# Performance work log

Measured on AMD Instinct MI355X. Metric: run time of the kernel, lower is better.

## Reference

```python
import jax, jax.numpy as jnp
import numpy as np

B, S, D = 4, 2048, 512
QKD = 256
HID = 3 * D  # expansion_factor=3
EPS = 1e-5


def _ln(x, g, b):
    m = jnp.mean(x, axis=-1, keepdims=True)
    v = jnp.mean((x - m) ** 2, axis=-1, keepdims=True)
    return (x - m) * jax.lax.rsqrt(v + EPS) * g + b


def setup_inputs() -> dict:
    key = jax.random.key(0)
    ks = jax.random.split(key, 12)
    s = lambda fan: 1.0 / np.sqrt(fan)
    return {
        "x":  jax.random.normal(ks[0], (B, S, D), jnp.float32),
        "Wm": jax.random.uniform(ks[1], (D, D), jnp.float32, -s(D), s(D)),
        "bm": jnp.zeros((D,), jnp.float32),
        "g1": jnp.ones((D,), jnp.float32),
        "b1": jnp.zeros((D,), jnp.float32),
        "Wh": jax.random.uniform(ks[2], (2 * HID, D), jnp.float32, -s(D), s(D)),
        "bh": jnp.zeros((2 * HID,), jnp.float32),
        "Wq": jax.random.uniform(ks[3], (QKD, D), jnp.float32, -s(D), s(D)),
        "bq": jnp.zeros((QKD,), jnp.float32),
        "Wb": jax.random.normal(ks[4], (QKD, QKD), jnp.float32),
        "Wo": jax.random.uniform(ks[5], (D, HID), jnp.float32, -s(HID), s(HID)),
        "bo": jnp.zeros((D,), jnp.float32),
        "g2": jnp.ones((D,), jnp.float32),
        "b2": jnp.zeros((D,), jnp.float32),
    }


def reference(x, Wm, bm, g1, b1, Wh, bh, Wq, bq, Wb, Wo, bo, g2, b2):
    seq_len = x.shape[-2]
    memory = jnp.einsum('bsd,ed->bse', x, Wm) + bm
    normed = _ln(x + memory, g1, b1)
    h = jax.nn.relu(jnp.einsum('bsd,hd->bsh', normed, Wh) + bh)
    v, gate = h[..., :HID], h[..., HID:]
    Z = jax.nn.relu(jnp.einsum('bsd,qd->bsq', normed, Wq) + bq)  # [B,S,QKD]
    QK = jnp.einsum('bid,de,bje->bij', Z, Wb, Z) / seq_len
    A = jax.nn.relu(QK) ** 2  # relu^2 attention, no softmax
    V = jnp.einsum('bij,bjd->bid', A, v) * gate
    out = _ln(jnp.einsum('bsh,dh->bsd', V, Wo) + bo, g2, b2)
    return out + x
```

## Files before the change

kernel.cpp:

```cpp
#include <hip/hip_runtime.h>

typedef unsigned short u16;
typedef unsigned char u8;
typedef __attribute__((ext_vector_type(8))) short short8;
typedef __attribute__((ext_vector_type(4))) float f32x4;

#define LN_EPS 1e-5f
#define SCALE_A 4096.f
#define SCALE_V 8.f
#define INV_SCALE_AV (1.f/32768.f)

__device__ __forceinline__ u16 f2bf(float f){
    union { float f; unsigned u; } c; c.f = f;
    unsigned u = c.u + 0x7FFFu + ((c.u >> 16) & 1u);
    return (u16)(u >> 16);
}
__device__ __forceinline__ float bf2f(u16 h){
    union { unsigned u; float f; } c; c.u = ((unsigned)h) << 16;
    return c.f;
}
__device__ __forceinline__ u8 f2fp8(float f){
    int r = __builtin_amdgcn_cvt_pk_fp8_f32(f, 0.f, 0, false);
    return (u8)(r & 0xFF);
}

enum { EPI_NONE=0, EPI_BIAS_RELU, EPI_RELUSQ, EPI_HSPLIT };
enum { OT_F32=0, OT_BF16=1, OT_FP8=2 };

__device__ __forceinline__ void gl2lds16(const void* g, void* lds){
    __builtin_amdgcn_global_load_lds(
        (const __attribute__((address_space(1))) unsigned*)g,
        (__attribute__((address_space(3))) unsigned*)lds, 16, 0, 0);
}

template<int EPI, int OT>
__global__ __launch_bounds__(256)
void mgemm(const u16* __restrict__ A, const u16* __restrict__ B, void* __restrict__ Cv,
           int K, int lda, int ldb, int ldc,
           long sAb, long sBb, long sCb,
           const float* __restrict__ bias,
           const void* __restrict__ ext, int ldext, long sEb,
           float scale, u16* __restrict__ out2, int hsplit)
{
    __shared__ u16 sA[2][4096];
    __shared__ u16 sB[2][4096];
    const int tid = threadIdx.x;
    const int m0 = blockIdx.y * 128, n0 = blockIdx.x * 128;
    const int z  = blockIdx.z;
    const u16* Az = A + (size_t)z * sAb;
    const u16* Bz = B + (size_t)z * sBb;

    const int lane = tid & 63, quad = lane >> 4, l15 = lane & 15;
    const int wave = tid >> 6;
    const int wm = (wave >> 1) * 64, wn = (wave & 1) * 64;

    const u16* gA[2]; const u16* gB[2]; int lo[2];
#pragma unroll
    for (int r = 0; r < 2; r++){
        const int c = tid + r * 256;
        gA[r] = Az + (size_t)(m0 + (c & 127)) * lda + (c >> 7) * 8;
        gB[r] = Bz + (size_t)(n0 + (c & 127)) * ldb + (c >> 7) * 8;
        lo[r] = ((tid & 192) + r * 256) * 16;
    }

    auto stage = [&](int buf, int k0){
#pragma unroll
        for (int r = 0; r < 2; r++){
            gl2lds16(gA[r] + k0, (char*)sA[buf] + lo[r]);
            gl2lds16(gB[r] + k0, (char*)sB[buf] + lo[r]);
        }
    };

    f32x4 acc[4][4];
#pragma unroll
    for (int i = 0; i < 4; i++)
#pragma unroll
        for (int j = 0; j < 4; j++) acc[i][j] = (f32x4){0.f,0.f,0.f,0.f};

    stage(0, 0);
    int buf = 0;
    for (int k0 = 0; k0 < K; k0 += 32){
        __syncthreads();
        if (k0 + 32 < K) stage(buf ^ 1, k0 + 32);
        const u16* fA = sA[buf] + quad * 1024 + (wm + l15) * 8;
        const u16* fB = sB[buf] + quad * 1024 + (wn + l15) * 8;
        short8 a[4], b[4];
#pragma unroll
        for (int t = 0; t < 4; t++){
            a[t] = *(const short8*)(fA + t * 128);
            b[t] = *(const short8*)(fB + t * 128);
        }
#pragma unroll
        for (int i = 0; i < 4; i++)
#pragma unroll
            for (int j = 0; j < 4; j++)
                acc[i][j] = __builtin_amdgcn_mfma_f32_16x16x32_bf16(a[i], b[j], acc[i][j], 0, 0, 0);
        buf ^= 1;
    }

    float* Cf = (float*)Cv; u16* Ch = (u16*)Cv; u8* C8 = (u8*)Cv;
    const size_t zc = (size_t)z * sCb;
#pragma unroll
    for (int i = 0; i < 4; i++){
#pragma unroll
        for (int j = 0; j < 4; j++){
            const int n = n0 + wn + j * 16 + l15;
            float bs = 0.f;
            if (EPI==EPI_BIAS_RELU || EPI==EPI_HSPLIT) bs = bias[n];
#pragma unroll
            for (int r = 0; r < 4; r++){
                const int m = m0 + wm + i * 16 + quad * 4 + r;
                float v = acc[i][j][r] + bs;
                if (EPI==EPI_BIAS_RELU || EPI==EPI_HSPLIT) v = fmaxf(v, 0.f);
                if (EPI==EPI_RELUSQ){ float t = fmaxf(v * scale, 0.f); v = t * t * SCALE_A; }
                if (EPI==EPI_HSPLIT){
                    if (n < hsplit) C8[(size_t)m * ldc + n] = f2fp8(v * SCALE_V);
                    else            out2[(size_t)m * ldc + n - hsplit] = f2bf(v);
                } else if (OT==OT_FP8){
                    C8[zc + (size_t)m * ldc + n] = f2fp8(v);
                } else if (OT==OT_BF16){
                    Ch[zc + (size_t)m * ldc + n] = f2bf(v);
                } else {
                    Cf[zc + (size_t)m * ldc + n] = v;
                }
            }
        }
    }
}

__global__ __launch_bounds__(256)
void mgemm8(const u8* __restrict__ A, const u8* __restrict__ B, u16* __restrict__ C,
            int K, int lda, int ldb, int ldc,
            long sAb, long sBb, long sCb,
            const u16* __restrict__ gate, int ldext, long sEb)
{
    __shared__ u8 sA[2][8192];
    __shared__ u8 sB[2][8192];
    const int tid = threadIdx.x;
    const int m0 = blockIdx.y * 128, n0 = blockIdx.x * 128;
    const int z  = blockIdx.z;
    const u8* Az = A + (size_t)z * sAb;
    const u8* Bz = B + (size_t)z * sBb;

    const int lane = tid & 63, quad = lane >> 4, l15 = lane & 15;
    const int wave = tid >> 6;
    const int wm = (wave >> 1) * 64, wn = (wave & 1) * 64;

    const u8* gA[2]; const u8* gB[2]; int lo[2];
#pragma unroll
    for (int r = 0; r < 2; r++){
        const int c = tid + r * 256;
        gA[r] = Az + (size_t)(m0 + (c & 127)) * lda + (c >> 7) * 16;
        gB[r] = Bz + (size_t)(n0 + (c & 127)) * ldb + (c >> 7) * 16;
        lo[r] = ((tid & 192) + r * 256) * 16;
    }

    auto stage = [&](int buf, int k0){
#pragma unroll
        for (int r = 0; r < 2; r++){
            gl2lds16(gA[r] + k0, (char*)sA[buf] + lo[r]);
            gl2lds16(gB[r] + k0, (char*)sB[buf] + lo[r]);
        }
    };

    f32x4 acc[4][4];
#pragma unroll
    for (int i = 0; i < 4; i++)
#pragma unroll
        for (int j = 0; j < 4; j++) acc[i][j] = (f32x4){0.f,0.f,0.f,0.f};

    stage(0, 0);
    int buf = 0;
    for (int k0 = 0; k0 < K; k0 += 64){
        __syncthreads();
        if (k0 + 64 < K) stage(buf ^ 1, k0 + 64);
#pragma unroll
        for (int t = 0; t < 2; t++){
            const u8* fA = sA[buf] + t * 4096 + (quad >> 1) * 2048 + (wm + l15) * 16 + (quad & 1) * 8;
            const u8* fB = sB[buf] + t * 4096 + (quad >> 1) * 2048 + (wn + l15) * 16 + (quad & 1) * 8;
            long a[4], b[4];
#pragma unroll
            for (int q = 0; q < 4; q++){
                a[q] = *(const long*)(fA + q * 256);
                b[q] = *(const long*)(fB + q * 256);
            }
#pragma unroll
            for (int i = 0; i < 4; i++)
#pragma unroll
                for (int j = 0; j < 4; j++)
                    acc[i][j] = __builtin_amdgcn_mfma_f32_16x16x32_fp8_fp8(a[i], b[j], acc[i][j], 0, 0, 0);
        }
        buf ^= 1;
    }

    const size_t zc = (size_t)z * sCb;
#pragma unroll
    for (int i = 0; i < 4; i++){
#pragma unroll
        for (int j = 0; j < 4; j++){
            const int n = n0 + wn + j * 16 + l15;
#pragma unroll
            for (int r = 0; r < 4; r++){
                const int m = m0 + wm + i * 16 + quad * 4 + r;
                float v = acc[i][j][r] * INV_SCALE_AV
                        * bf2f(gate[(size_t)z * sEb + (size_t)m * ldext + n]);
                C[zc + (size_t)m * ldc + n] = f2bf(v);
            }
        }
    }
}

template<bool OUT_BF, bool POST_RES, int NSUM, bool PRE_RES>
__global__ __launch_bounds__(256)
void ln_k(const float* __restrict__ in, const float* __restrict__ g,
          const float* __restrict__ b, const float* __restrict__ res_post,
          const float* __restrict__ res_pre, const float* __restrict__ bias2,
          long pstride, void* __restrict__ out)
{
    const int row = blockIdx.x, tid = threadIdx.x;
    const size_t base = (size_t)row * 512 + tid * 2;
    float2 v = *(const float2*)(in + base);
#pragma unroll
    for (int p = 1; p < NSUM; p++){
        const float2 w = *(const float2*)(in + (size_t)p * pstride + base);
        v.x += w.x; v.y += w.y;
    }
    if (NSUM > 1){
        const float2 bb2 = *(const float2*)(bias2 + tid * 2);
        v.x += bb2.x; v.y += bb2.y;
    }
    if (PRE_RES){
        const float2 r = *(const float2*)(res_pre + base);
        v.x += r.x; v.y += r.y;
    }
    float s = v.x + v.y, ss = v.x * v.x + v.y * v.y;
#pragma unroll
    for (int off = 32; off > 0; off >>= 1){
        s  += __shfl_down(s,  off);
        ss += __shfl_down(ss, off);
    }
    __shared__ float sbuf[8], ssbuf[8];
    const int wid = tid >> 6, lane = tid & 63;
    if (lane == 0){ sbuf[wid] = s; ssbuf[wid] = ss; }
    __syncthreads();
    if (tid == 0){
        float S = 0.f, SS = 0.f;
#pragma unroll
        for (int i = 0; i < 4; i++){ S += sbuf[i]; SS += ssbuf[i]; }
        const float mean = S * (1.f/512.f);
        const float var  = SS * (1.f/512.f) - mean * mean;
        sbuf[4]  = mean;
        ssbuf[4] = rsqrtf(var + LN_EPS);
    }
    __syncthreads();
    const float mean = sbuf[4], rstd = ssbuf[4];
    const float2 gg = *(const float2*)(g + tid * 2);
    const float2 bb = *(const float2*)(b + tid * 2);
    float ox = (v.x - mean) * rstd * gg.x + bb.x;
    float oy = (v.y - mean) * rstd * gg.y + bb.y;
    if (POST_RES){
        const float2 r = *(const float2*)(res_post + base);
        ox += r.x; oy += r.y;
    }
    if (OUT_BF){
        unsigned pk = ((unsigned)f2bf(oy) << 16) | (unsigned)f2bf(ox);
        ((unsigned*)out)[(size_t)row * 256 + tid] = pk;
    } else {
        *(float2*)((float*)out + base) = make_float2(ox, oy);
    }
}

__global__ __launch_bounds__(256)
void castall_k(const float* __restrict__ x, const float* __restrict__ Wm,
               const float* __restrict__ Wh, const float* __restrict__ Wq,
               const float* __restrict__ Wo, const float* __restrict__ Wb,
               u16* __restrict__ xb, u16* __restrict__ Wmb, u16* __restrict__ Whb,
               u16* __restrict__ Wqb, u16* __restrict__ Wob, u16* __restrict__ WbT)
{
    const int i = blockIdx.x * 256 + threadIdx.x;
    if (i >= 1736704){
        const int j = i - 1736704;
        if (j < 65536){
            const int e = j >> 8, d = j & 255;
            WbT[e * 256 + d] = f2bf(Wb[d * 256 + e]);
        }
        return;
    }
    const float* src; u16* dst; int off;
    if      (i < 1048576){ src = x;  dst = xb;  off = i; }
    else if (i < 1114112){ src = Wm; dst = Wmb; off = i - 1048576; }
    else if (i < 1507328){ src = Wh; dst = Whb; off = i - 1114112; }
    else if (i < 1540096){ src = Wq; dst = Wqb; off = i - 1507328; }
    else                 { src = Wo; dst = Wob; off = i - 1540096; }
    const float4 v = ((const float4*)src)[off];
    ushort4 o; o.x = f2bf(v.x); o.y = f2bf(v.y); o.z = f2bf(v.z); o.w = f2bf(v.w);
    ((ushort4*)dst)[off] = o;
}

__global__ __launch_bounds__(256)
void tr8_k(const u8* __restrict__ v, u8* __restrict__ vT, int S, int HID){
    const int b = blockIdx.z;
    const int h0 = blockIdx.x * 64, s0 = blockIdx.y * 64;
    __shared__ u8 t[64][68];
    const u8* vb = v + (size_t)b * S * HID;
    u8* vTb = vT + (size_t)b * HID * S;
    const int tid = threadIdx.x;
#pragma unroll
    for (int i = 0; i < 4; i++){
        int idx = tid + i * 256;
        int r = idx >> 4, c4 = (idx & 15) * 4;
        uchar4 u = *(const uchar4*)(vb + (size_t)(s0 + r) * HID + h0 + c4);
        t[r][c4] = u.x; t[r][c4+1] = u.y; t[r][c4+2] = u.z; t[r][c4+3] = u.w;
    }
    __syncthreads();
#pragma unroll
    for (int i = 0; i < 4; i++){
        int idx = tid + i * 256;
        int r = idx >> 4, c4 = (idx & 15) * 4;
        uchar4 u;
        u.x = t[c4][r]; u.y = t[c4+1][r]; u.z = t[c4+2][r]; u.w = t[c4+3][r];
        *(uchar4*)(vTb + (size_t)(h0 + r) * S + s0 + c4) = u;
    }
}

extern "C" void kernel_launch(void* const* d_in, const int* in_sizes, int n_in,
                              void* d_out, int out_size, void* d_ws, size_t ws_size,
                              hipStream_t stream)
{
    const float* x  = (const float*)d_in[0];
    const float* Wm = (const float*)d_in[1];
    const float* bm = (const float*)d_in[2];
    const float* g1 = (const float*)d_in[3];
    const float* b1 = (const float*)d_in[4];
    const float* Wh = (const float*)d_in[5];
    const float* bh = (const float*)d_in[6];
    const float* Wq = (const float*)d_in[7];
    const float* bq = (const float*)d_in[8];
    const float* Wb = (const float*)d_in[9];
    const float* Wo = (const float*)d_in[10];
    const float* bo = (const float*)d_in[11];
    const float* g2 = (const float*)d_in[12];
    const float* b2 = (const float*)d_in[13];
    float* out = (float*)d_out;
    (void)in_sizes; (void)n_in; (void)out_size; (void)ws_size;

    const int Bn=4, S=2048, D=512, QKD=256, HID=1536, H2=3072;
    const int M = Bn * S;
    const long MD = (long)M * D;

    char* p = (char*)d_ws;
    auto alloc = [&](size_t bytes)->void*{ void* r = p; p += (bytes + 255) & ~(size_t)255; return r; };
    u16*  xbf  = (u16*) alloc((size_t)M*D*2);
    u16*  Wmbf = (u16*) alloc((size_t)D*D*2);
    u16*  Whbf = (u16*) alloc((size_t)H2*D*2);
    u16*  Wqbf = (u16*) alloc((size_t)QKD*D*2);
    u16*  Wobf = (u16*) alloc((size_t)D*HID*2);
    u16*  WbT  = (u16*) alloc((size_t)QKD*QKD*2);
    float* ybuf= (float*)alloc((size_t)MD*4*3);
    u16*  Zb   = (u16*) alloc((size_t)M*QKD*2);
    u16*  ZWbb = (u16*) alloc((size_t)M*QKD*2);
    u8*   v8   = (u8*)  alloc((size_t)M*HID);
    u16*  gbf  = (u16*) alloc((size_t)M*HID*2);
    u8*   vT8  = (u8*)  alloc((size_t)M*HID);
    u8*   A8   = (u8*)  alloc((size_t)M*S);
    u16*  Vgbf = (u16*) alloc((size_t)M*HID*2);
    u16*  nrm  = xbf;

    dim3 blk(256);

    castall_k<<<dim3(7040), blk, 0, stream>>>(x, Wm, Wh, Wq, Wo, Wb,
                                              xbf, Wmbf, Whbf, Wqbf, Wobf, WbT);
    mgemm<EPI_NONE,OT_F32><<<dim3(D/128, M/128, 2), blk, 0, stream>>>(
        xbf, Wmbf, ybuf, D/2, D, D, D, 256, 256, MD,
        nullptr, nullptr, 0, 0, 1.f, nullptr, 0);
    ln_k<true,false,2,true><<<dim3(M), blk, 0, stream>>>(
        ybuf, g1, b1, nullptr, x, bm, MD, nrm);
    mgemm<EPI_HSPLIT,OT_FP8><<<dim3(H2/128, M/128, 1), blk, 0, stream>>>(
        nrm, Whbf, v8, D, D, D, HID, 0,0,0, bh, nullptr, 0, 0, 1.f, gbf, HID);
    mgemm<EPI_BIAS_RELU,OT_BF16><<<dim3(QKD/128, M/128, 1), blk, 0, stream>>>(
        nrm, Wqbf, Zb, D, D, D, QKD, 0,0,0, bq, nullptr, 0, 0, 1.f, nullptr, 0);
    mgemm<EPI_NONE,OT_BF16><<<dim3(QKD/128, M/128, 1), blk, 0, stream>>>(
        Zb, WbT, ZWbb, QKD, QKD, QKD, QKD, 0,0,0, nullptr, nullptr, 0, 0, 1.f, nullptr, 0);
    mgemm<EPI_RELUSQ,OT_FP8><<<dim3(S/128, S/128, Bn), blk, 0, stream>>>(
        ZWbb, Zb, A8, QKD, QKD, QKD, S,
        (long)S*QKD, (long)S*QKD, (long)S*S,
        nullptr, nullptr, 0, 0, 1.f/(float)S, nullptr, 0);
    tr8_k<<<dim3(HID/64, S/64, Bn), blk, 0, stream>>>(v8, vT8, S, HID);
    mgemm8<<<dim3(HID/128, S/128, Bn), blk, 0, stream>>>(
        A8, vT8, Vgbf, S, S, S, HID,
        (long)S*S, (long)HID*S, (long)S*HID,
        gbf, HID, (long)S*HID);
    mgemm<EPI_NONE,OT_F32><<<dim3(D/128, M/128, 3), blk, 0, stream>>>(
        Vgbf, Wobf, ybuf, HID/3, HID, HID, D, 512, 512, MD,
        nullptr, nullptr, 0, 0, 1.f, nullptr, 0);
    ln_k<false,true,3,false><<<dim3(M), blk, 0, stream>>>(
        ybuf, g2, b2, x, nullptr, bo, MD, out);
}
```

Baseline: 377.0 us.

## Use MX-scaled fp8 MFMA for AV GEMM, fuse Wh/Wq GEMMs, drop split-K

The A·V GEMM now uses the gfx950 scaled 16x16x128 f8f6f4 MFMA with unit scales. It loads 128-wide K tiles into XOR-swizzled LDS, single-buffered with two barriers per iteration. The Wh and Wq projections are merged into one dual-output kernel launch. The memory GEMM drops split-K and folds bias and residual into its epilogue, so the first LayerNorm reads a single partial. These changes aim to raise MFMA throughput and cut launches and partial-sum traffic, at the cost of losing load/compute overlap in the AV kernel and lower parallelism in the memory GEMM.

```diff
diff --git a/kernel.cpp b/kernel.cpp
--- a/kernel.cpp
+++ b/kernel.cpp
@@ -4,11 +4,14 @@
 typedef unsigned char u8;
 typedef __attribute__((ext_vector_type(8))) short short8;
 typedef __attribute__((ext_vector_type(4))) float f32x4;
+typedef __attribute__((ext_vector_type(8))) int int8v;
+typedef __attribute__((ext_vector_type(4))) int int4v;
 
 #define LN_EPS 1e-5f
 #define SCALE_A 4096.f
 #define SCALE_V 8.f
 #define INV_SCALE_AV (1.f/32768.f)
+#define MX_ONE 0x7F7F7F7Fu
 
 __device__ __forceinline__ u16 f2bf(float f){
     union { float f; unsigned u; } c; c.f = f;
@@ -24,7 +27,7 @@
     return (u8)(r & 0xFF);
 }
 
-enum { EPI_NONE=0, EPI_BIAS_RELU, EPI_RELUSQ, EPI_HSPLIT };
+enum { EPI_NONE=0, EPI_BIAS_RES, EPI_RELUSQ };
 enum { OT_F32=0, OT_BF16=1, OT_FP8=2 };
 
 __device__ __forceinline__ void gl2lds16(const void* g, void* lds){
@@ -39,8 +42,8 @@
            int K, int lda, int ldb, int ldc,
            long sAb, long sBb, long sCb,
            const float* __restrict__ bias,
-           const void* __restrict__ ext, int ldext, long sEb,
-           float scale, u16* __restrict__ out2, int hsplit)
+           const float* __restrict__ ext, int ldext,
+           float scale)
 {
     __shared__ u16 sA[2][4096];
     __shared__ u16 sB[2][4096];
@@ -105,37 +108,111 @@
 #pragma unroll
         for (int j = 0; j < 4; j++){
             const int n = n0 + wn + j * 16 + l15;
-            float bs = 0.f;
-            if (EPI==EPI_BIAS_RELU || EPI==EPI_HSPLIT) bs = bias[n];
+            float bs = (EPI==EPI_BIAS_RES) ? bias[n] : 0.f;
 #pragma unroll
             for (int r = 0; r < 4; r++){
                 const int m = m0 + wm + i * 16 + quad * 4 + r;
                 float v = acc[i][j][r] + bs;
-                if (EPI==EPI_BIAS_RELU || EPI==EPI_HSPLIT) v = fmaxf(v, 0.f);
+                if (EPI==EPI_BIAS_RES)
+                    v += ext[(size_t)m * ldext + n];
                 if (EPI==EPI_RELUSQ){ float t = fmaxf(v * scale, 0.f); v = t * t * SCALE_A; }
-                if (EPI==EPI_HSPLIT){
-                    if (n < hsplit) C8[(size_t)m * ldc + n] = f2fp8(v * SCALE_V);
-                    else            out2[(size_t)m * ldc + n - hsplit] = f2bf(v);
-                } else if (OT==OT_FP8){
-                    C8[zc + (size_t)m * ldc + n] = f2fp8(v);
-                } else if (OT==OT_BF16){
-                    Ch[zc + (size_t)m * ldc + n] = f2bf(v);
-                } else {
-                    Cf[zc + (size_t)m * ldc + n] = v;
-                }
+                if (OT==OT_FP8)       C8[zc + (size_t)m * ldc + n] = f2fp8(v);
+                else if (OT==OT_BF16) Ch[zc + (size_t)m * ldc + n] = f2bf(v);
+                else                  Cf[zc + (size_t)m * ldc + n] = v;
             }
         }
     }
 }
 
 __global__ __launch_bounds__(256)
-void mgemm8(const u8* __restrict__ A, const u8* __restrict__ B, u16* __restrict__ C,
-            int K, int lda, int ldb, int ldc,
-            long sAb, long sBb, long sCb,
-            const u16* __restrict__ gate, int ldext, long sEb)
-{
-    __shared__ u8 sA[2][8192];
-    __shared__ u8 sB[2][8192];
+void mgemm_dual(const u16* __restrict__ Anrm, const u16* __restrict__ Wh,
+                const u16* __restrict__ Wq,
+                const float* __restrict__ bh, const float* __restrict__ bq,
+                u8* __restrict__ v8, u16* __restrict__ gbf, u16* __restrict__ Zb)
+{
+    __shared__ u16 sA[2][4096];
+    __shared__ u16 sB[2][4096];
+    const int tid = threadIdx.x;
+    const bool isZ = blockIdx.x >= 24;
+    const u16* Bm = isZ ? Wq : Wh;
+    const float* bias = isZ ? bq : bh;
+    const int m0 = blockIdx.y * 128;
+    const int n0 = (isZ ? (blockIdx.x - 24) : blockIdx.x) * 128;
+    const int K = 512, lda = 512, ldb = 512;
+
+    const int lane = tid & 63, quad = lane >> 4, l15 = lane & 15;
+    const int wave = tid >> 6;
+    const int wm = (wave >> 1) * 64, wn = (wave & 1) * 64;
+
+    const u16* gA[2]; const u16* gB[2]; int lo[2];
+#pragma unroll
+    for (int r = 0; r < 2; r++){
+        const int c = tid + r * 256;
+        gA[r] = Anrm + (size_t)(m0 + (c & 127)) * lda + (c >> 7) * 8;
+        gB[r] = Bm   + (size_t)(n0 + (c & 127)) * ldb + (c >> 7) * 8;
+        lo[r] = ((tid & 192) + r * 256) * 16;
+    }
+    auto stage = [&](int buf, int k0){
+#pragma unroll
+        for (int r = 0; r < 2; r++){
+            gl2lds16(gA[r] + k0, (char*)sA[buf] + lo[r]);
+            gl2lds16(gB[r] + k0, (char*)sB[buf] + lo[r]);
+        }
+    };
+
+    f32x4 acc[4][4];
+#pragma unroll
+    for (int i = 0; i < 4; i++)
+#pragma unroll
+        for (int j = 0; j < 4; j++) acc[i][j] = (f32x4){0.f,0.f,0.f,0.f};
+
+    stage(0, 0);
+    int buf = 0;
+    for (int k0 = 0; k0 < K; k0 += 32){
+        __syncthreads();
+        if (k0 + 32 < K) stage(buf ^ 1, k0 + 32);
+        const u16* fA = sA[buf] + quad * 1024 + (wm + l15) * 8;
+        const u16* fB = sB[buf] + quad * 1024 + (wn + l15) * 8;
+        short8 a[4], b[4];
+#pragma unroll
+        for (int t = 0; t < 4; t++){
+            a[t] = *(const short8*)(fA + t * 128);
+            b[t] = *(const short8*)(fB + t * 128);
+        }
+#pragma unroll
+        for (int i = 0; i < 4; i++)
+#pragma unroll
+            for (int j = 0; j < 4; j++)
+                acc[i][j] = __builtin_amdgcn_mfma_f32_16x16x32_bf16(a[i], b[j], acc[i][j], 0, 0, 0);
+        buf ^= 1;
+    }
+
+#pragma unroll
+    for (int i = 0; i < 4; i++){
+#pragma unroll
+        for (int j = 0; j < 4; j++){
+            const int n = n0 + wn + j * 16 + l15;
+            const float bs = bias[n];
+#pragma unroll
+            for (int r = 0; r < 4; r++){
+                const int m = m0 + wm + i * 16 + quad * 4 + r;
+                float v = fmaxf(acc[i][j][r] + bs, 0.f);
+                if (isZ)            Zb[(size_t)m * 256 + n] = f2bf(v);
+                else if (n < 1536)  v8[(size_t)m * 1536 + n] = f2fp8(v * SCALE_V);
+                else                gbf[(size_t)m * 1536 + n - 1536] = f2bf(v);
+            }
+        }
+    }
+}
+
+__global__ __launch_bounds__(256)
+void mgemm8mx(const u8* __restrict__ A, const u8* __restrict__ B, u16* __restrict__ C,
+              int K, int lda, int ldb, int ldc,
+              long sAb, long sBb, long sCb,
+              const u16* __restrict__ gate, int ldext, long sEb)
+{
+    __shared__ u8 sA[16384];
+    __shared__ u8 sB[16384];
     const int tid = threadIdx.x;
     const int m0 = blockIdx.y * 128, n0 = blockIdx.x * 128;
     const int z  = blockIdx.z;
@@ -146,22 +223,15 @@
     const int wave = tid >> 6;
     const int wm = (wave >> 1) * 64, wn = (wave & 1) * 64;
 
-    const u8* gA[2]; const u8* gB[2]; int lo[2];
-#pragma unroll
-    for (int r = 0; r < 2; r++){
-        const int c = tid + r * 256;
-        gA[r] = Az + (size_t)(m0 + (c & 127)) * lda + (c >> 7) * 16;
-        gB[r] = Bz + (size_t)(n0 + (c & 127)) * ldb + (c >> 7) * 16;
-        lo[r] = ((tid & 192) + r * 256) * 16;
-    }
-
-    auto stage = [&](int buf, int k0){
-#pragma unroll
-        for (int r = 0; r < 2; r++){
-            gl2lds16(gA[r] + k0, (char*)sA[buf] + lo[r]);
-            gl2lds16(gB[r] + k0, (char*)sB[buf] + lo[r]);
-        }
-    };
+    const u8* gA[4]; const u8* gB[4]; int lo[4];
+#pragma unroll
+    for (int p = 0; p < 4; p++){
+        const int r = p * 32 + (tid >> 3);
+        const int j = (tid & 7) ^ (r & 7);
+        gA[p] = Az + (size_t)(m0 + r) * lda + j * 16;
+        gB[p] = Bz + (size_t)(n0 + r) * ldb + j * 16;
+        lo[p] = p * 4096 + wave * 1024;
+    }
 
     f32x4 acc[4][4];
 #pragma unroll
@@ -169,28 +239,32 @@
 #pragma unroll
         for (int j = 0; j < 4; j++) acc[i][j] = (f32x4){0.f,0.f,0.f,0.f};
 
-    stage(0, 0);
-    int buf = 0;
-    for (int k0 = 0; k0 < K; k0 += 64){
+    for (int k0 = 0; k0 < K; k0 += 128){
+#pragma unroll
+        for (int p = 0; p < 4; p++){
+            gl2lds16(gA[p] + k0, (char*)sA + lo[p]);
+            gl2lds16(gB[p] + k0, (char*)sB + lo[p]);
+        }
         __syncthreads();
-        if (k0 + 64 < K) stage(buf ^ 1, k0 + 64);
-#pragma unroll
-        for (int t = 0; t < 2; t++){
-            const u8* fA = sA[buf] + t * 4096 + (quad >> 1) * 2048 + (wm + l15) * 16 + (quad & 1) * 8;
-            const u8* fB = sB[buf] + t * 4096 + (quad >> 1) * 2048 + (wn + l15) * 16 + (quad & 1) * 8;
-            long a[4], b[4];
-#pragma unroll
-            for (int q = 0; q < 4; q++){
-                a[q] = *(const long*)(fA + q * 256);
-                b[q] = *(const long*)(fB + q * 256);
-            }
-#pragma unroll
-            for (int i = 0; i < 4; i++)
-#pragma unroll
-                for (int j = 0; j < 4; j++)
-                    acc[i][j] = __builtin_amdgcn_mfma_f32_16x16x32_fp8_fp8(a[i], b[j], acc[i][j], 0, 0, 0);
-        }
-        buf ^= 1;
+        int8v a[4], b[4];
+#pragma unroll
+        for (int i = 0; i < 4; i++){
+            const int m = wm + i * 16 + l15;
+            const int4v a0 = *(const int4v*)(sA + m * 128 + ((2*quad    ) ^ (m & 7)) * 16);
+            const int4v a1 = *(const int4v*)(sA + m * 128 + ((2*quad + 1) ^ (m & 7)) * 16);
+            a[i] = (int8v){a0[0],a0[1],a0[2],a0[3],a1[0],a1[1],a1[2],a1[3]};
+            const int n = wn + i * 16 + l15;
+            const int4v b0 = *(const int4v*)(sB + n * 128 + ((2*quad    ) ^ (n & 7)) * 16);
+            const int4v b1 = *(const int4v*)(sB + n * 128 + ((2*quad + 1) ^ (n & 7)) * 16);
+            b[i] = (int8v){b0[0],b0[1],b0[2],b0[3],b1[0],b1[1],b1[2],b1[3]};
+        }
+#pragma unroll
+        for (int i = 0; i < 4; i++)
+#pragma unroll
+            for (int j = 0; j < 4; j++)
+                acc[i][j] = __builtin_amdgcn_mfma_scale_f32_16x16x128_f8f6f4(
+                    a[i], b[j], acc[i][j], 0, 0, 0, MX_ONE, 0, MX_ONE);
+        __syncthreads();
     }
 
     const size_t zc = (size_t)z * sCb;
@@ -370,29 +444,26 @@
 
     castall_k<<<dim3(7040), blk, 0, stream>>>(x, Wm, Wh, Wq, Wo, Wb,
                                               xbf, Wmbf, Whbf, Wqbf, Wobf, WbT);
-    mgemm<EPI_NONE,OT_F32><<<dim3(D/128, M/128, 2), blk, 0, stream>>>(
-        xbf, Wmbf, ybuf, D/2, D, D, D, 256, 256, MD,
-        nullptr, nullptr, 0, 0, 1.f, nullptr, 0);
-    ln_k<true,false,2,true><<<dim3(M), blk, 0, stream>>>(
-        ybuf, g1, b1, nullptr, x, bm, MD, nrm);
-    mgemm<EPI_HSPLIT,OT_FP8><<<dim3(H2/128, M/128, 1), blk, 0, stream>>>(
-        nrm, Whbf, v8, D, D, D, HID, 0,0,0, bh, nullptr, 0, 0, 1.f, gbf, HID);
-    mgemm<EPI_BIAS_RELU,OT_BF16><<<dim3(QKD/128, M/128, 1), blk, 0, stream>>>(
-        nrm, Wqbf, Zb, D, D, D, QKD, 0,0,0, bq, nullptr, 0, 0, 1.f, nullptr, 0);
+    mgemm<EPI_BIAS_RES,OT_F32><<<dim3(D/128, M/128, 1), blk, 0, stream>>>(
+        xbf, Wmbf, ybuf, D, D, D, D, 0,0,0, bm, x, D, 1.f);
+    ln_k<true,false,1,false><<<dim3(M), blk, 0, stream>>>(
+        ybuf, g1, b1, nullptr, nullptr, nullptr, 0, nrm);
+    mgemm_dual<<<dim3(26, M/128), blk, 0, stream>>>(
+        nrm, Whbf, Wqbf, bh, bq, v8, gbf, Zb);
     mgemm<EPI_NONE,OT_BF16><<<dim3(QKD/128, M/128, 1), blk, 0, stream>>>(
-        Zb, WbT, ZWbb, QKD, QKD, QKD, QKD, 0,0,0, nullptr, nullptr, 0, 0, 1.f, nullptr, 0);
+        Zb, WbT, ZWbb, QKD, QKD, QKD, QKD, 0,0,0, nullptr, nullptr, 0, 1.f);
     mgemm<EPI_RELUSQ,OT_FP8><<<dim3(S/128, S/128, Bn), blk, 0, stream>>>(
         ZWbb, Zb, A8, QKD, QKD, QKD, S,
         (long)S*QKD, (long)S*QKD, (long)S*S,
-        nullptr, nullptr, 0, 0, 1.f/(float)S, nullptr, 0);
+        nullptr, nullptr, 0, 1.f/(float)S);
     tr8_k<<<dim3(HID/64, S/64, Bn), blk, 0, stream>>>(v8, vT8, S, HID);
-    mgemm8<<<dim3(HID/128, S/128, Bn), blk, 0, stream>>>(
+    mgemm8mx<<<dim3(HID/128, S/128, Bn), blk, 0, stream>>>(
         A8, vT8, Vgbf, S, S, S, HID,
         (long)S*S, (long)HID*S, (long)S*HID,
         gbf, HID, (long)S*HID);
     mgemm<EPI_NONE,OT_F32><<<dim3(D/128, M/128, 3), blk, 0, stream>>>(
         Vgbf, Wobf, ybuf, HID/3, HID, HID, D, 512, 512, MD,
-        nullptr, nullptr, 0, 0, 1.f, nullptr, 0);
+        nullptr, nullptr, 0, 1.f);
     ln_k<false,true,3,false><<<dim3(M), blk, 0, stream>>>(
         ybuf, g2, b2, x, nullptr, bo, MD, out);
 }
```

New measurement: 341.7 us. 9.4% less time.
